# Optimization experiments

Hardware: AMD Instinct MI355X
Metric: run time of the kernel (lower is better)

## Reference

```python
import jax, jax.numpy as jnp
import numpy as np

N = 100000   # nodes
D = 64       # padded neighbor-list width (avg degree)
F = 256      # in_channels
H = 256      # hidden_channels
E = 131072   # number of target edges
OUT = 1      # out_channels


def _linear_params(key, fin, fout):
    k1, k2 = jax.random.split(key)
    s = 1.0 / np.sqrt(fin)
    w = jax.random.uniform(k1, (fin, fout), jnp.float32, -s, s)
    b = jax.random.uniform(k2, (fout,), jnp.float32, -s, s)
    return w, b


def setup_inputs() -> dict:
    key = jax.random.key(0)
    ks = jax.random.split(key, 12)
    x = jax.random.normal(ks[0], (N, F), jnp.float32)
    # sorted padded neighbor lists: row i -> D neighbor ids (sorted, as in the
    # bit-packed sorted-element representation the torch code intersects)
    neighbors = jnp.sort(jax.random.randint(ks[1], (N, D), 0, N), axis=1).astype(jnp.int32)
    tar_ei = jax.random.randint(ks[2], (2, E), 0, N).astype(jnp.int32)
    cn_w1, cn_b1 = _linear_params(ks[3], 1, H)
    cn_w2, cn_b2 = _linear_params(ks[4], H, H)
    cn_w3, cn_b3 = _linear_params(ks[5], H, H)
    ij_w1, ij_b1 = _linear_params(ks[6], F, H)
    ij_w2, ij_b2 = _linear_params(ks[7], H, H)
    lin_w1, lin_b1 = _linear_params(ks[8], H, H)
    lin_w2, lin_b2 = _linear_params(ks[9], H, OUT)
    beta = jnp.ones((1,), jnp.float32)
    return dict(x=x, neighbors=neighbors, tar_ei=tar_ei, beta=beta,
                cn_w1=cn_w1, cn_b1=cn_b1, cn_w2=cn_w2, cn_b2=cn_b2,
                cn_w3=cn_w3, cn_b3=cn_b3,
                ij_w1=ij_w1, ij_b1=ij_b1, ij_w2=ij_w2, ij_b2=ij_b2,
                lin_w1=lin_w1, lin_b1=lin_b1, lin_w2=lin_w2, lin_b2=lin_b2)


def reference(x, neighbors, tar_ei, beta,
              cn_w1, cn_b1, cn_w2, cn_b2, cn_w3, cn_b3,
              ij_w1, ij_b1, ij_w2, ij_b2,
              lin_w1, lin_b1, lin_w2, lin_b2):
    src, dst = tar_ei[0], tar_ei[1]
    xi = x[src]                       # [E, F] irregular gather
    xj = x[dst]                       # [E, F]

    # adjoverlap / spmoverlap_: per edge, |N(i) ∩ N(j)| via sorted-set
    # intersection; cn.sum(dim=-1) with fill value 1.0 -> CN count.
    ni = neighbors[src]               # [E, D]
    nj = neighbors[dst]               # [E, D]
    matches = ni[:, :, None] == nj[:, None, :]          # [E, D, D]
    xcn = jnp.sum(matches, axis=(1, 2)).astype(jnp.float32)[:, None]  # [E, 1]

    # xcnlin: Linear(1,H) -> ReLU -> Linear(H,H) -> ReLU -> Linear(H,H)
    h = jax.nn.relu(xcn @ cn_w1 + cn_b1)
    h = jax.nn.relu(h @ cn_w2 + cn_b2)
    xcn_feat = h @ cn_w3 + cn_b3                         # [E, H]

    # xijlin: Linear(F,H) -> ReLU -> Linear(H,H)
    g = jax.nn.relu((xi * xj) @ ij_w1 + ij_b1)
    xij = g @ ij_w2 + ij_b2                              # [E, H]

    # lin: Linear(H,H) -> ReLU -> Linear(H,OUT)
    z = jax.nn.relu((xcn_feat * beta + xij) @ lin_w1 + lin_b1)
    out = z @ lin_w2 + lin_b2                            # [E, OUT]
    return out
```

## Files before the change

### kernel.cpp

```cpp
#include <hip/hip_runtime.h>
#include <hip/hip_bf16.h>
#include <stdint.h>

#define EE 131072
#define DDEG 64

typedef __bf16 bf16_t;
typedef bf16_t bf16x8 __attribute__((ext_vector_type(8)));
typedef float floatx4 __attribute__((ext_vector_type(4)));

#define SWZ(row, k) (((row) << 8) + ((k) ^ (((row) & 7) << 3)))

__global__ __launch_bounds__(256)
void prep_kernel(const float* __restrict__ x, bf16_t* __restrict__ xb,
                 const float* __restrict__ ij_w1, bf16_t* __restrict__ Wt1,
                 const float* __restrict__ w2, const float* __restrict__ lw1,
                 bf16_t* __restrict__ Mt,
                 const float* __restrict__ b2, const float* __restrict__ lb1,
                 float* __restrict__ cvec,
                 const float* __restrict__ cw1, const float* __restrict__ cb1,
                 const float* __restrict__ cw2, const float* __restrict__ cb2,
                 const float* __restrict__ cw3, const float* __restrict__ cb3,
                 const float* __restrict__ beta, float* __restrict__ T2) {
    __shared__ __align__(16) char arena[33792];
    const int bid = blockIdx.x;
    const int t = threadIdx.x;

    if (bid >= 1088) {
        size_t base = (size_t)(bid - 1088) * 4096 + (size_t)t * 16;
        float4 a0 = *(const float4*)(x + base);
        float4 a1 = *(const float4*)(x + base + 4);
        float4 a2 = *(const float4*)(x + base + 8);
        float4 a3 = *(const float4*)(x + base + 12);
        bf16x8 o0, o1;
        o0[0] = (bf16_t)a0.x; o0[1] = (bf16_t)a0.y; o0[2] = (bf16_t)a0.z; o0[3] = (bf16_t)a0.w;
        o0[4] = (bf16_t)a1.x; o0[5] = (bf16_t)a1.y; o0[6] = (bf16_t)a1.z; o0[7] = (bf16_t)a1.w;
        o1[0] = (bf16_t)a2.x; o1[1] = (bf16_t)a2.y; o1[2] = (bf16_t)a2.z; o1[3] = (bf16_t)a2.w;
        o1[4] = (bf16_t)a3.x; o1[5] = (bf16_t)a3.y; o1[6] = (bf16_t)a3.z; o1[7] = (bf16_t)a3.w;
        *(bf16x8*)(xb + base)     = o0;
        *(bf16x8*)(xb + base + 8) = o1;
        return;
    }

    if (bid < 64) {
        float (*tile)[33] = (float (*)[33])arena;
        int bx = bid & 7, by = bid >> 3;
        int tx = t & 31, ty = t >> 5;
        #pragma unroll
        for (int r = 0; r < 32; r += 8)
            tile[ty + r][tx] = ij_w1[(by * 32 + ty + r) * 256 + bx * 32 + tx];
        __syncthreads();
        #pragma unroll
        for (int r = 0; r < 32; r += 8)
            Wt1[(bx * 32 + ty + r) * 256 + by * 32 + tx] = (bf16_t)tile[tx][ty + r];
    } else if (bid < 320) {
        float (*S)[33] = (float (*)[33])arena;
        int b = bid - 64;
        int cc = t & 31, abase = t >> 5;
        float acc = 0.f;
        for (int c0 = 0; c0 < 256; c0 += 32) {
            __syncthreads();
            #pragma unroll
            for (int r = 0; r < 32; ++r) {
                int a = r * 8 + abase;
                S[a][cc] = w2[a * 256 + c0 + cc];
            }
            __syncthreads();
            #pragma unroll 8
            for (int c2 = 0; c2 < 32; ++c2) {
                float wv = lw1[(c0 + c2) * 256 + b];
                acc += S[t][c2] * wv;
            }
        }
        Mt[(size_t)b * 256 + t] = (bf16_t)acc;
    } else if (bid < 576) {
        float* red = (float*)arena;
        int b = bid - 320;
        red[t] = b2[t] * lw1[t * 256 + b];
        __syncthreads();
        for (int s = 128; s > 0; s >>= 1) {
            if (t < s) red[t] += red[t + s];
            __syncthreads();
        }
        if (t == 0) cvec[b] = red[0] + lb1[b];
    } else {
        float* t1 = (float*)arena;
        float* t2 = (float*)(arena + 1024);
        float* t3 = (float*)(arena + 2048);
        int v = bid - 576;
        float fv = (float)v;
        t1[t] = fmaxf(fv * cw1[t] + cb1[t], 0.f);
        __syncthreads();
        float s = cb2[t];
        for (int k = 0; k < 256; ++k) s += t1[k] * cw2[k * 256 + t];
        t2[t] = fmaxf(s, 0.f);
        __syncthreads();
        s = cb3[t];
        for (int k = 0; k < 256; ++k) s += t2[k] * cw3[k * 256 + t];
        t3[t] = s * beta[0];
        __syncthreads();
        s = 0.f;
        for (int k = 0; k < 256; ++k) s += t3[k] * lw1[k * 256 + t];
        T2[(size_t)v * 256 + t] = s;
    }
}

__global__ __launch_bounds__(256, 3)
void fused_kernel(const bf16_t* __restrict__ xb, const int* __restrict__ tar,
                  const int* __restrict__ nbr,
                  const bf16_t* __restrict__ Wt1, const float* __restrict__ b1,
                  const bf16_t* __restrict__ Mt, const float* __restrict__ cvec,
                  const float* __restrict__ T2,
                  const float* __restrict__ w2, const float* __restrict__ b2s,
                  float* __restrict__ out) {
    __shared__ __align__(16) bf16_t X[64 * 256];
    __shared__ float rowacc[64];
    __shared__ int xcn_s[64];

    const int tid  = threadIdx.x;
    const int lane = tid & 63;
    const int wc   = tid >> 6;
    const int quad = lane >> 4;
    const int l16  = lane & 15;
    const int e0   = blockIdx.x * 64;

    int va[16], vb[16];
    #pragma unroll
    for (int i = 0; i < 16; ++i) {
        int e = e0 + wc * 16 + i;
        int s = __builtin_amdgcn_readfirstlane(tar[e]);
        int d = __builtin_amdgcn_readfirstlane(tar[EE + e]);
        va[i] = nbr[(size_t)s * DDEG + lane];
        vb[i] = nbr[(size_t)d * DDEG + lane];
    }

    {
        const int srow   = tid >> 2;
        const int skbase = (tid & 3) * 8;
        int e = e0 + srow;
        const bf16_t* xi = xb + (size_t)tar[e] * 256 + skbase;
        const bf16_t* xj = xb + (size_t)tar[EE + e] * 256 + skbase;
        bf16x8 ui[8], vj[8];
        #pragma unroll
        for (int kc = 0; kc < 8; ++kc) {
            ui[kc] = *(const bf16x8*)(xi + kc * 32);
            vj[kc] = *(const bf16x8*)(xj + kc * 32);
        }
        #pragma unroll
        for (int kc = 0; kc < 8; ++kc) {
            bf16x8 p;
            #pragma unroll
            for (int m = 0; m < 8; ++m)
                p[m] = (bf16_t)((float)ui[kc][m] * (float)vj[kc][m]);
            *(bf16x8*)&X[SWZ(srow, kc * 32 + skbase)] = p;
        }
    }

    __syncthreads();

    #pragma unroll
    for (int p = 0; p < 8; ++p) {
        int cpk = 0;
        #pragma unroll
        for (int h = 0; h < 2; ++h) {
            int i = p * 2 + h;
            int lo = 0, hi = 0;
            #pragma unroll
            for (int st = 32; st; st >>= 1) {
                int bl = __shfl(vb[i], lo + st - 1, 64);
                int bh = __shfl(vb[i], hi + st - 1, 64);
                lo += (bl < va[i]) ? st : 0;
                hi += (bh <= va[i]) ? st : 0;
            }
            int b63 = __shfl(vb[i], 63, 64);
            lo += (b63 < va[i]) ? 1 : 0;
            hi += (b63 <= va[i]) ? 1 : 0;
            cpk += (hi - lo) << (16 * h);
        }
        #pragma unroll
        for (int off = 32; off; off >>= 1) cpk += __shfl_xor(cpk, off, 64);
        if (lane == 0) {
            int c0 = cpk & 0xffff, c1 = (int)((unsigned)cpk >> 16);
            xcn_s[wc * 16 + p * 2]     = c0 < 511 ? c0 : 511;
            xcn_s[wc * 16 + p * 2 + 1] = c1 < 511 ? c1 : 511;
        }
    }

    floatx4 acc[4][4];
    #pragma unroll
    for (int i = 0; i < 4; ++i)
        #pragma unroll
        for (int j = 0; j < 4; ++j)
            acc[i][j] = (floatx4){0.f, 0.f, 0.f, 0.f};

    #pragma unroll 2
    for (int kc = 0; kc < 8; ++kc) {
        const int k0 = kc * 32 + quad * 8;
        bf16x8 af[4], bfr[4];
        #pragma unroll
        for (int j = 0; j < 4; ++j)
            bfr[j] = *(const bf16x8*)(Wt1 + (size_t)(wc * 64 + j * 16 + l16) * 256 + k0);
        #pragma unroll
        for (int i = 0; i < 4; ++i)
            af[i] = *(const bf16x8*)(&X[SWZ(i * 16 + l16, k0)]);
        #pragma unroll
        for (int i = 0; i < 4; ++i)
            #pragma unroll
            for (int j = 0; j < 4; ++j)
                acc[i][j] = __builtin_amdgcn_mfma_f32_16x16x32_bf16(
                                af[i], bfr[j], acc[i][j], 0, 0, 0);
    }

    __syncthreads();

    #pragma unroll
    for (int j = 0; j < 4; ++j) {
        int col  = wc * 64 + j * 16 + l16;
        float bv = b1[col];
        #pragma unroll
        for (int i = 0; i < 4; ++i)
            #pragma unroll
            for (int r = 0; r < 4; ++r) {
                int row = i * 16 + quad * 4 + r;
                X[SWZ(row, col)] = (bf16_t)fmaxf(acc[i][j][r] + bv, 0.f);
            }
    }
    #pragma unroll
    for (int i = 0; i < 4; ++i)
        #pragma unroll
        for (int j = 0; j < 4; ++j)
            acc[i][j] = (floatx4){0.f, 0.f, 0.f, 0.f};
    if (tid < 64) rowacc[tid] = 0.f;

    __syncthreads();

    #pragma unroll 2
    for (int kc = 0; kc < 8; ++kc) {
        const int k0 = kc * 32 + quad * 8;
        bf16x8 af[4], bfr[4];
        #pragma unroll
        for (int j = 0; j < 4; ++j)
            bfr[j] = *(const bf16x8*)(Mt + (size_t)(wc * 64 + j * 16 + l16) * 256 + k0);
        #pragma unroll
        for (int i = 0; i < 4; ++i)
            af[i] = *(const bf16x8*)(&X[SWZ(i * 16 + l16, k0)]);
        #pragma unroll
        for (int i = 0; i < 4; ++i)
            #pragma unroll
            for (int j = 0; j < 4; ++j)
                acc[i][j] = __builtin_amdgcn_mfma_f32_16x16x32_bf16(
                                af[i], bfr[j], acc[i][j], 0, 0, 0);
    }

    int xv[16];
    #pragma unroll
    for (int i = 0; i < 4; ++i)
        #pragma unroll
        for (int r = 0; r < 4; ++r)
            xv[i * 4 + r] = xcn_s[i * 16 + quad * 4 + r];

    float pr[16];
    #pragma unroll
    for (int t = 0; t < 16; ++t) pr[t] = 0.f;
    #pragma unroll
    for (int j = 0; j < 4; ++j) {
        int col  = wc * 64 + j * 16 + l16;
        float cv = cvec[col];
        float wv = w2[col];
        #pragma unroll
        for (int i = 0; i < 4; ++i)
            #pragma unroll
            for (int r = 0; r < 4; ++r) {
                float t2v = T2[(size_t)xv[i * 4 + r] * 256 + col];
                float v = fmaxf(acc[i][j][r] + cv + t2v, 0.f);
                pr[i * 4 + r] += v * wv;
            }
    }
    #pragma unroll
    for (int off = 1; off < 16; off <<= 1)
        #pragma unroll
        for (int t = 0; t < 16; ++t)
            pr[t] += __shfl_xor(pr[t], off, 64);
    if (l16 == 0) {
        #pragma unroll
        for (int i = 0; i < 4; ++i)
            #pragma unroll
            for (int r = 0; r < 4; ++r)
                atomicAdd(&rowacc[i * 16 + quad * 4 + r], pr[i * 4 + r]);
    }
    __syncthreads();
    if (tid < 64) out[e0 + tid] = rowacc[tid] + b2s[0];
}

extern "C" void kernel_launch(void* const* d_in, const int* in_sizes, int n_in,
                              void* d_out, int out_size, void* d_ws, size_t ws_size,
                              hipStream_t stream) {
    const float* x      = (const float*)d_in[0];
    const int*   nbr    = (const int*)  d_in[1];
    const int*   tar    = (const int*)  d_in[2];
    const float* beta   = (const float*)d_in[3];
    const float* cn_w1  = (const float*)d_in[4];
    const float* cn_b1  = (const float*)d_in[5];
    const float* cn_w2  = (const float*)d_in[6];
    const float* cn_b2  = (const float*)d_in[7];
    const float* cn_w3  = (const float*)d_in[8];
    const float* cn_b3  = (const float*)d_in[9];
    const float* ij_w1  = (const float*)d_in[10];
    const float* ij_b1  = (const float*)d_in[11];
    const float* ij_w2  = (const float*)d_in[12];
    const float* ij_b2  = (const float*)d_in[13];
    const float* lin_w1 = (const float*)d_in[14];
    const float* lin_b1 = (const float*)d_in[15];
    const float* lin_w2 = (const float*)d_in[16];
    const float* lin_b2 = (const float*)d_in[17];

    char* ws = (char*)d_ws;
    float*  T2    = (float*) (ws + 0);
    bf16_t* Wt1   = (bf16_t*)(ws + 1048576);
    bf16_t* Mt    = (bf16_t*)(ws + 1179648);
    float*  cvec  = (float*) (ws + 1310720);
    bf16_t* xb    = (bf16_t*)(ws + 1312768);

    prep_kernel<<<1088 + 6250, 256, 0, stream>>>(
        x, xb, ij_w1, Wt1, ij_w2, lin_w1, Mt,
        ij_b2, lin_b1, cvec,
        cn_w1, cn_b1, cn_w2, cn_b2, cn_w3, cn_b3, beta, T2);
    fused_kernel<<<EE / 64, 256, 0, stream>>>(xb, tar, nbr, Wt1, ij_b1, Mt, cvec,
                                              T2, lin_w2, lin_b2,
                                              (float*)d_out);
}
```

Baseline: 313.3 us.

## Gather fp32 node features directly and drop the separate bf16 conversion pass

Removes the prep-kernel blocks that converted all of x to bf16 in a workspace buffer. The fused kernel now gathers fp32 rows of x per edge and multiplies them in fp32 before rounding to bf16. This trades a full read and write of x for twice the bytes per gathered row. It also raises the occupancy hint from 3 to 5 blocks, moves the per-edge common-neighbour counts from shared memory to a global workspace buffer, and replaces the shared-memory atomic row reduction with a per-wave partial write plus a summed readout.

```diff
diff --git a/kernel.cpp b/kernel.cpp
--- a/kernel.cpp
+++ b/kernel.cpp
@@ -12,8 +12,7 @@
 #define SWZ(row, k) (((row) << 8) + ((k) ^ (((row) & 7) << 3)))
 
 __global__ __launch_bounds__(256)
-void prep_kernel(const float* __restrict__ x, bf16_t* __restrict__ xb,
-                 const float* __restrict__ ij_w1, bf16_t* __restrict__ Wt1,
+void prep_kernel(const float* __restrict__ ij_w1, bf16_t* __restrict__ Wt1,
                  const float* __restrict__ w2, const float* __restrict__ lw1,
                  bf16_t* __restrict__ Mt,
                  const float* __restrict__ b2, const float* __restrict__ lb1,
@@ -26,22 +25,6 @@
     const int bid = blockIdx.x;
     const int t = threadIdx.x;
 
-    if (bid >= 1088) {
-        size_t base = (size_t)(bid - 1088) * 4096 + (size_t)t * 16;
-        float4 a0 = *(const float4*)(x + base);
-        float4 a1 = *(const float4*)(x + base + 4);
-        float4 a2 = *(const float4*)(x + base + 8);
-        float4 a3 = *(const float4*)(x + base + 12);
-        bf16x8 o0, o1;
-        o0[0] = (bf16_t)a0.x; o0[1] = (bf16_t)a0.y; o0[2] = (bf16_t)a0.z; o0[3] = (bf16_t)a0.w;
-        o0[4] = (bf16_t)a1.x; o0[5] = (bf16_t)a1.y; o0[6] = (bf16_t)a1.z; o0[7] = (bf16_t)a1.w;
-        o1[0] = (bf16_t)a2.x; o1[1] = (bf16_t)a2.y; o1[2] = (bf16_t)a2.z; o1[3] = (bf16_t)a2.w;
-        o1[4] = (bf16_t)a3.x; o1[5] = (bf16_t)a3.y; o1[6] = (bf16_t)a3.z; o1[7] = (bf16_t)a3.w;
-        *(bf16x8*)(xb + base)     = o0;
-        *(bf16x8*)(xb + base + 8) = o1;
-        return;
-    }
-
     if (bid < 64) {
         float (*tile)[33] = (float (*)[33])arena;
         int bx = bid & 7, by = bid >> 3;
@@ -105,17 +88,15 @@
     }
 }
 
-__global__ __launch_bounds__(256, 3)
-void fused_kernel(const bf16_t* __restrict__ xb, const int* __restrict__ tar,
+__global__ __launch_bounds__(256, 5)
+void fused_kernel(const float* __restrict__ x, const int* __restrict__ tar,
                   const int* __restrict__ nbr,
                   const bf16_t* __restrict__ Wt1, const float* __restrict__ b1,
                   const bf16_t* __restrict__ Mt, const float* __restrict__ cvec,
-                  const float* __restrict__ T2,
+                  const float* __restrict__ T2, int* __restrict__ xcnbuf,
                   const float* __restrict__ w2, const float* __restrict__ b2s,
                   float* __restrict__ out) {
     __shared__ __align__(16) bf16_t X[64 * 256];
-    __shared__ float rowacc[64];
-    __shared__ int xcn_s[64];
 
     const int tid  = threadIdx.x;
     const int lane = tid & 63;
@@ -135,24 +116,32 @@
     }
 
     {
-        const int srow   = tid >> 2;
-        const int skbase = (tid & 3) * 8;
+        const int srow = tid >> 2;
+        const int kb   = (tid & 3) * 64;
         int e = e0 + srow;
-        const bf16_t* xi = xb + (size_t)tar[e] * 256 + skbase;
-        const bf16_t* xj = xb + (size_t)tar[EE + e] * 256 + skbase;
-        bf16x8 ui[8], vj[8];
-        #pragma unroll
-        for (int kc = 0; kc < 8; ++kc) {
-            ui[kc] = *(const bf16x8*)(xi + kc * 32);
-            vj[kc] = *(const bf16x8*)(xj + kc * 32);
-        }
-        #pragma unroll
-        for (int kc = 0; kc < 8; ++kc) {
-            bf16x8 p;
-            #pragma unroll
-            for (int m = 0; m < 8; ++m)
-                p[m] = (bf16_t)((float)ui[kc][m] * (float)vj[kc][m]);
-            *(bf16x8*)&X[SWZ(srow, kc * 32 + skbase)] = p;
+        const float* xi = x + (size_t)tar[e] * 256 + kb;
+        const float* xj = x + (size_t)tar[EE + e] * 256 + kb;
+        #pragma unroll
+        for (int c = 0; c < 4; ++c) {
+            float4 a0 = *(const float4*)(xi + c * 16);
+            float4 a1 = *(const float4*)(xi + c * 16 + 4);
+            float4 a2 = *(const float4*)(xi + c * 16 + 8);
+            float4 a3 = *(const float4*)(xi + c * 16 + 12);
+            float4 b0 = *(const float4*)(xj + c * 16);
+            float4 b1v = *(const float4*)(xj + c * 16 + 4);
+            float4 b2v = *(const float4*)(xj + c * 16 + 8);
+            float4 b3 = *(const float4*)(xj + c * 16 + 12);
+            bf16x8 p0, p1;
+            p0[0] = (bf16_t)(a0.x * b0.x);  p0[1] = (bf16_t)(a0.y * b0.y);
+            p0[2] = (bf16_t)(a0.z * b0.z);  p0[3] = (bf16_t)(a0.w * b0.w);
+            p0[4] = (bf16_t)(a1.x * b1v.x); p0[5] = (bf16_t)(a1.y * b1v.y);
+            p0[6] = (bf16_t)(a1.z * b1v.z); p0[7] = (bf16_t)(a1.w * b1v.w);
+            p1[0] = (bf16_t)(a2.x * b2v.x); p1[1] = (bf16_t)(a2.y * b2v.y);
+            p1[2] = (bf16_t)(a2.z * b2v.z); p1[3] = (bf16_t)(a2.w * b2v.w);
+            p1[4] = (bf16_t)(a3.x * b3.x);  p1[5] = (bf16_t)(a3.y * b3.y);
+            p1[6] = (bf16_t)(a3.z * b3.z);  p1[7] = (bf16_t)(a3.w * b3.w);
+            *(bf16x8*)&X[SWZ(srow, kb + c * 16)]     = p0;
+            *(bf16x8*)&X[SWZ(srow, kb + c * 16 + 8)] = p1;
         }
     }
 
@@ -181,8 +170,8 @@
         for (int off = 32; off; off >>= 1) cpk += __shfl_xor(cpk, off, 64);
         if (lane == 0) {
             int c0 = cpk & 0xffff, c1 = (int)((unsigned)cpk >> 16);
-            xcn_s[wc * 16 + p * 2]     = c0 < 511 ? c0 : 511;
-            xcn_s[wc * 16 + p * 2 + 1] = c1 < 511 ? c1 : 511;
+            xcnbuf[e0 + wc * 16 + p * 2]     = c0 < 511 ? c0 : 511;
+            xcnbuf[e0 + wc * 16 + p * 2 + 1] = c1 < 511 ? c1 : 511;
         }
     }
 
@@ -230,7 +219,6 @@
         #pragma unroll
         for (int j = 0; j < 4; ++j)
             acc[i][j] = (floatx4){0.f, 0.f, 0.f, 0.f};
-    if (tid < 64) rowacc[tid] = 0.f;
 
     __syncthreads();
 
@@ -257,7 +245,7 @@
     for (int i = 0; i < 4; ++i)
         #pragma unroll
         for (int r = 0; r < 4; ++r)
-            xv[i * 4 + r] = xcn_s[i * 16 + quad * 4 + r];
+            xv[i * 4 + r] = xcnbuf[e0 + i * 16 + quad * 4 + r];
 
     float pr[16];
     #pragma unroll
@@ -281,15 +269,20 @@
         #pragma unroll
         for (int t = 0; t < 16; ++t)
             pr[t] += __shfl_xor(pr[t], off, 64);
+
+    __syncthreads();
+    float* red = (float*)X;
     if (l16 == 0) {
         #pragma unroll
         for (int i = 0; i < 4; ++i)
             #pragma unroll
             for (int r = 0; r < 4; ++r)
-                atomicAdd(&rowacc[i * 16 + quad * 4 + r], pr[i * 4 + r]);
-    }
-    __syncthreads();
-    if (tid < 64) out[e0 + tid] = rowacc[tid] + b2s[0];
+                red[wc * 64 + i * 16 + quad * 4 + r] = pr[i * 4 + r];
+    }
+    __syncthreads();
+    if (tid < 64)
+        out[e0 + tid] = red[tid] + red[64 + tid] + red[128 + tid]
+                      + red[192 + tid] + b2s[0];
 }
 
 extern "C" void kernel_launch(void* const* d_in, const int* in_sizes, int n_in,
@@ -315,17 +308,17 @@
     const float* lin_b2 = (const float*)d_in[17];
 
     char* ws = (char*)d_ws;
-    float*  T2    = (float*) (ws + 0);
-    bf16_t* Wt1   = (bf16_t*)(ws + 1048576);
-    bf16_t* Mt    = (bf16_t*)(ws + 1179648);
-    float*  cvec  = (float*) (ws + 1310720);
-    bf16_t* xb    = (bf16_t*)(ws + 1312768);
-
-    prep_kernel<<<1088 + 6250, 256, 0, stream>>>(
-        x, xb, ij_w1, Wt1, ij_w2, lin_w1, Mt,
+    float*  T2     = (float*) (ws + 0);
+    bf16_t* Wt1    = (bf16_t*)(ws + 1048576);
+    bf16_t* Mt     = (bf16_t*)(ws + 1179648);
+    float*  cvec   = (float*) (ws + 1310720);
+    int*    xcnbuf = (int*)   (ws + 1312768);
+
+    prep_kernel<<<1088, 256, 0, stream>>>(
+        ij_w1, Wt1, ij_w2, lin_w1, Mt,
         ij_b2, lin_b1, cvec,
         cn_w1, cn_b1, cn_w2, cn_b2, cn_w3, cn_b3, beta, T2);
-    fused_kernel<<<EE / 64, 256, 0, stream>>>(xb, tar, nbr, Wt1, ij_b1, Mt, cvec,
-                                              T2, lin_w2, lin_b2,
+    fused_kernel<<<EE / 64, 256, 0, stream>>>(x, tar, nbr, Wt1, ij_b1, Mt, cvec,
+                                              T2, xcnbuf, lin_w2, lin_b2,
                                               (float*)d_out);
 }
```

Result: slower. 449.6 us (+43.5%).
